# Performance work log

Measured on AMD Instinct MI355X. Metric: run time of the kernel, lower is better.

Reference implementation:

```python
import jax, jax.numpy as jnp
import numpy as np

N_NODES = 50000
N_EDGES = 1600000
D = 128


def _degree_norm(idx, n_nodes, dtype):
    # unweighted degree, clamped to >= 1, power -1/2 (DGL norm='both')
    deg = jax.ops.segment_sum(jnp.ones((idx.shape[0],), dtype=dtype), idx,
                              num_segments=n_nodes)
    return jax.lax.rsqrt(jnp.maximum(deg, 1.0))


def _graph_conv(h, e_weight, src, dst, W, b, out_norm, in_norm):
    # DGL GraphConv, norm='both', aggregate-first (in_feats == out_feats)
    feat_src = h * out_norm[:, None]                     # [N, D]
    msg = feat_src[src] * e_weight[:, None]              # [E, D] gather + edge weight
    agg = jax.ops.segment_sum(msg, dst, num_segments=h.shape[0])  # [N, D] scatter-add
    agg = agg * in_norm[:, None]
    return jax.nn.relu(agg @ W + b)


def setup_inputs() -> dict:
    key = jax.random.key(0)
    ks = jax.random.split(key, 6)
    x = jax.random.normal(ks[0], (N_NODES, D), dtype=jnp.float32)
    e_weight = jax.random.uniform(ks[1], (N_EDGES,), dtype=jnp.float32)
    src = jax.random.randint(ks[2], (N_EDGES,), 0, N_NODES)
    dst = jax.random.randint(ks[3], (N_EDGES,), 0, N_NODES)
    scale = 1.0 / np.sqrt(D)
    W1 = jax.random.normal(ks[4], (D, D), dtype=jnp.float32) * scale
    W2 = jax.random.normal(ks[5], (D, D), dtype=jnp.float32) * scale
    b1 = jnp.zeros((D,), dtype=jnp.float32)
    b2 = jnp.zeros((D,), dtype=jnp.float32)
    return {"x": x, "e_weight": e_weight, "src": src, "dst": dst,
            "W1": W1, "b1": b1, "W2": W2, "b2": b2}


def reference(x, e_weight, src, dst, W1, b1, W2, b2):
    n = x.shape[0]
    out_norm = _degree_norm(src, n, x.dtype)  # src -> out-degree norm
    in_norm = _degree_norm(dst, n, x.dtype)   # dst -> in-degree norm
    h = x
    for W, b in ((W1, b1), (W2, b2)):
        h_nxt = _graph_conv(h, e_weight, src, dst, W, b, out_norm, in_norm)
        h = h_nxt + h  # residual=1, dims match
    return h
```

## Files before the change

kernel.cpp:

```cpp
#include <hip/hip_runtime.h>

static constexpr int NN = 50000;
static constexpr int NE = 1600000;
static constexpr int DD = 128;
static constexpr int STRIDE = 72;
static constexpr int NBUCK = 196;
static constexpr int CAP = 9000;
static constexpr int B1B = 512;
static constexpr int CHUNK = NE / B1B;
static constexpr int SCAN_BLOCKS = (NN + 255) / 256;

typedef __attribute__((ext_vector_type(8))) short short8;
typedef __attribute__((ext_vector_type(4))) float f32x4;

__device__ inline unsigned short f2b(float f) {
    unsigned u = __float_as_uint(f);
    return (unsigned short)((u + 0x7FFFu + ((u >> 16) & 1u)) >> 16);
}
__device__ inline float b2f(unsigned short h) {
    return __uint_as_float(((unsigned)h) << 16);
}
__device__ inline unsigned pack2(float lo, float hi) {
    return (unsigned)f2b(lo) | ((unsigned)f2b(hi) << 16);
}
__device__ inline void acc8(float* a, uint4 r, float w) {
    a[0] = fmaf(__uint_as_float(r.x << 16), w, a[0]);
    a[1] = fmaf(__uint_as_float(r.x & 0xFFFF0000u), w, a[1]);
    a[2] = fmaf(__uint_as_float(r.y << 16), w, a[2]);
    a[3] = fmaf(__uint_as_float(r.y & 0xFFFF0000u), w, a[3]);
    a[4] = fmaf(__uint_as_float(r.z << 16), w, a[4]);
    a[5] = fmaf(__uint_as_float(r.z & 0xFFFF0000u), w, a[5]);
    a[6] = fmaf(__uint_as_float(r.w << 16), w, a[6]);
    a[7] = fmaf(__uint_as_float(r.w & 0xFFFF0000u), w, a[7]);
}


__global__ __launch_bounds__(256) void build1_kernel(
    const int* __restrict__ src, const int* __restrict__ dst,
    const float* __restrict__ ew,
    int* __restrict__ gCurD, int* __restrict__ gCurS,
    uint2* __restrict__ tempD, unsigned short* __restrict__ tempS) {
    __shared__ int lsrc[CHUNK];
    __shared__ int ldst[CHUNK];
    __shared__ int histD[NBUCK * 2], histS[NBUCK * 2];
    __shared__ int baseD[NBUCK], baseS[NBUCK];
    int tid = threadIdx.x;
    int cp = tid & 1;
    for (int i = tid; i < NBUCK; i += 256) {
        histD[i * 2] = 0; histD[i * 2 + 1] = 0;
        histS[i * 2] = 0; histS[i * 2 + 1] = 0;
    }
    int lo = blockIdx.x * CHUNK;
    for (int i = tid; i < CHUNK; i += 256) {
        lsrc[i] = src[lo + i];
        ldst[i] = dst[lo + i];
    }
    __syncthreads();
    for (int i = tid; i < CHUNK; i += 256) {
        atomicAdd(&histD[(ldst[i] >> 8) * 2 + cp], 1);
        atomicAdd(&histS[(lsrc[i] >> 8) * 2 + cp], 1);
    }
    __syncthreads();
    for (int i = tid; i < NBUCK; i += 256) {
        int d0 = histD[i * 2], d1 = histD[i * 2 + 1];
        baseD[i] = atomicAdd(&gCurD[i], d0 + d1);
        histD[i * 2] = 0; histD[i * 2 + 1] = d0;
        int s0 = histS[i * 2], s1 = histS[i * 2 + 1];
        baseS[i] = atomicAdd(&gCurS[i], s0 + s1);
        histS[i * 2] = 0; histS[i * 2 + 1] = s0;
    }
    __syncthreads();
    for (int i = tid; i < CHUNK; i += 256) {
        int s = lsrc[i], d = ldst[i];
        unsigned short wb = f2b(ew[lo + i]);
        int bd = d >> 8, bs = s >> 8;
        int pd = baseD[bd] + atomicAdd(&histD[bd * 2 + cp], 1);
        if (pd < CAP) tempD[(size_t)bd * CAP + pd] = make_uint2(((unsigned)s << 16) | wb, (unsigned)d);
        int ps = baseS[bs] + atomicAdd(&histS[bs * 2 + cp], 1);
        if (ps < CAP) tempS[(size_t)bs * CAP + ps] = (unsigned short)(s & 255);
    }
}

__global__ __launch_bounds__(512) void build2_kernel(
    const unsigned short* __restrict__ tempS, const int* __restrict__ gCurS,
    const uint2* __restrict__ tempD, const int* __restrict__ gCurD,
    const float* __restrict__ x, float* __restrict__ onorm,
    unsigned short* __restrict__ xs,
    unsigned* __restrict__ edges, int* __restrict__ cnt_in,
    float* __restrict__ inorm,
    const float* __restrict__ W1, const float* __restrict__ W2,
    unsigned short* __restrict__ Wt1, unsigned short* __restrict__ Wt2) {
    __shared__ int cur[256];
    __shared__ float on[256];
    int tid = threadIdx.x, b = blockIdx.x;

    if (b < NBUCK) {
        if (tid < 256) cur[tid] = 0;
        __syncthreads();
        int n = min(gCurS[b], CAP);
        const unsigned short* rec = tempS + (size_t)b * CAP;
        for (int i = tid; i < n; i += 512) atomicAdd(&cur[rec[i]], 1);
        __syncthreads();
        if (tid < 256) {
            int node = (b << 8) + tid;
            float o = rsqrtf(fmaxf((float)cur[tid], 1.0f));
            on[tid] = o;
            if (node < NN) onorm[node] = o;
        }
        __syncthreads();
        #pragma unroll
        for (int k = 0; k < 8; ++k) {
            int t = tid + (k << 9);
            int r = t >> 4, sub = t & 15;
            int node = (b << 8) + r;
            if (node >= NN) continue;
            const float4* xv = (const float4*)(x + (size_t)node * DD + sub * 8);
            float o = on[r];
            float4 a = xv[0], c = xv[1];
            uint4 oo;
            oo.x = pack2(a.x * o, a.y * o);
            oo.y = pack2(a.z * o, a.w * o);
            oo.z = pack2(c.x * o, c.y * o);
            oo.w = pack2(c.z * o, c.w * o);
            ((uint4*)xs)[(size_t)node * 16 + sub] = oo;
        }
    } else if (b < 2 * NBUCK) {
        int bb = b - NBUCK;
        if (tid < 256) cur[tid] = 0;
        __syncthreads();
        int n = min(gCurD[bb], CAP);
        const uint2* rec = tempD + (size_t)bb * CAP;
        for (int i = tid; i < n; i += 512) {
            uint2 r = rec[i];
            int d = (int)r.y;
            int slot = atomicAdd(&cur[d & 255], 1);
            if (slot < STRIDE) edges[(size_t)d * STRIDE + slot] = r.x;
        }
        __syncthreads();
        if (tid < 256) {
            int node = (bb << 8) + tid;
            if (node < NN) {
                int c = cur[tid];
                cnt_in[node] = min(c, STRIDE);
                inorm[node] = rsqrtf(fmaxf((float)c, 1.0f));
            }
        }
    } else {
        for (int idx = tid; idx < 2 * 16384; idx += 512) {
            const float* Ws = (idx < 16384) ? W1 : W2;
            unsigned short* Wd = (idx < 16384) ? Wt1 : Wt2;
            int i = idx & 16383;
            int k = i >> 7, n = i & 127;
            Wd[n * 128 + k] = f2b(Ws[i]);
        }
    }
}

template<bool WRITE_HS>
__global__ __launch_bounds__(256) void fused_kernel(
    const unsigned short* __restrict__ hsrc, const unsigned* __restrict__ edges,
    const int* __restrict__ cnt, const unsigned short* __restrict__ Wt,
    const float* __restrict__ bias, const float* __restrict__ inorm,
    const float* __restrict__ onorm, const float* __restrict__ hres,
    float* __restrict__ out, unsigned short* __restrict__ hs) {
    __shared__ uint4 lsA[256];

    int tid = threadIdx.x;
    int node0 = blockIdx.x * 16;

    {
        int nl = tid >> 4;
        int lane = tid & 15;
        int node = node0 + nl;
        int n = cnt[node];
        const uint4* rows = (const uint4*)hsrc;
        const unsigned* ep = edges + node * STRIDE;
        float acc[8] = {0.f,0.f,0.f,0.f,0.f,0.f,0.f,0.f};
        int i = 0;
        for (; i + 8 <= n; i += 8) {
            uint4 ea = *(const uint4*)(ep + i);
            uint4 eb = *(const uint4*)(ep + i + 4);
            uint4 r0 = rows[(ea.x >> 16) * 16 + lane];
            uint4 r1 = rows[(ea.y >> 16) * 16 + lane];
            uint4 r2 = rows[(ea.z >> 16) * 16 + lane];
            uint4 r3 = rows[(ea.w >> 16) * 16 + lane];
            uint4 r4 = rows[(eb.x >> 16) * 16 + lane];
            uint4 r5 = rows[(eb.y >> 16) * 16 + lane];
            uint4 r6 = rows[(eb.z >> 16) * 16 + lane];
            uint4 r7 = rows[(eb.w >> 16) * 16 + lane];
            acc8(acc, r0, b2f((unsigned short)(ea.x & 0xFFFFu)));
            acc8(acc, r1, b2f((unsigned short)(ea.y & 0xFFFFu)));
            acc8(acc, r2, b2f((unsigned short)(ea.z & 0xFFFFu)));
            acc8(acc, r3, b2f((unsigned short)(ea.w & 0xFFFFu)));
            acc8(acc, r4, b2f((unsigned short)(eb.x & 0xFFFFu)));
            acc8(acc, r5, b2f((unsigned short)(eb.y & 0xFFFFu)));
            acc8(acc, r6, b2f((unsigned short)(eb.z & 0xFFFFu)));
            acc8(acc, r7, b2f((unsigned short)(eb.w & 0xFFFFu)));
        }
        if (i + 4 <= n) {
            uint4 ea = *(const uint4*)(ep + i);
            uint4 r0 = rows[(ea.x >> 16) * 16 + lane];
            uint4 r1 = rows[(ea.y >> 16) * 16 + lane];
            uint4 r2 = rows[(ea.z >> 16) * 16 + lane];
            uint4 r3 = rows[(ea.w >> 16) * 16 + lane];
            acc8(acc, r0, b2f((unsigned short)(ea.x & 0xFFFFu)));
            acc8(acc, r1, b2f((unsigned short)(ea.y & 0xFFFFu)));
            acc8(acc, r2, b2f((unsigned short)(ea.z & 0xFFFFu)));
            acc8(acc, r3, b2f((unsigned short)(ea.w & 0xFFFFu)));
            i += 4;
        }
        for (; i < n; ++i) {
            unsigned wrd = ep[i];
            uint4 r = rows[(wrd >> 16) * 16 + lane];
            acc8(acc, r, b2f((unsigned short)(wrd & 0xFFFFu)));
        }
        uint4 p;
        p.x = pack2(acc[0], acc[1]);
        p.y = pack2(acc[2], acc[3]);
        p.z = pack2(acc[4], acc[5]);
        p.w = pack2(acc[6], acc[7]);
        lsA[nl * 16 + (lane ^ nl)] = p;
    }
    __syncthreads();

    int l = tid & 63;
    int w = tid >> 6;
    int r16 = l & 15;
    int q = l >> 4;

    const short8* lsAs = (const short8*)lsA;
    short8 afrag[4];
    #pragma unroll
    for (int kk = 0; kk < 4; ++kk) {
        int chunk = kk * 4 + q;
        afrag[kk] = lsAs[r16 * 16 + (chunk ^ r16)];
    }

    int col0 = w * 32 + r16;
    int col1 = col0 + 16;
    const uint4* wt4 = (const uint4*)Wt;
    f32x4 acc0 = {0.f, 0.f, 0.f, 0.f};
    f32x4 acc1 = {0.f, 0.f, 0.f, 0.f};
    #pragma unroll
    for (int kk = 0; kk < 4; ++kk) {
        int cidx = kk * 4 + q;
        uint4 bu0 = wt4[col0 * 16 + cidx];
        uint4 bu1 = wt4[col1 * 16 + cidx];
        short8 b0 = *(const short8*)&bu0;
        short8 b1 = *(const short8*)&bu1;
        acc0 = __builtin_amdgcn_mfma_f32_16x16x32_bf16(afrag[kk], b0, acc0, 0, 0, 0);
        acc1 = __builtin_amdgcn_mfma_f32_16x16x32_bf16(afrag[kk], b1, acc1, 0, 0, 0);
    }

    float bc0 = bias[col0], bc1 = bias[col1];
    #pragma unroll
    for (int reg = 0; reg < 4; ++reg) {
        int row = q * 4 + reg;
        int n = node0 + row;
        float inr = inorm[n];
        size_t o0 = (size_t)n * DD + col0;
        size_t o1 = (size_t)n * DD + col1;
        float v0 = fmaxf(fmaf(acc0[reg], inr, bc0), 0.0f) + hres[o0];
        float v1 = fmaxf(fmaf(acc1[reg], inr, bc1), 0.0f) + hres[o1];
        out[o0] = v0;
        out[o1] = v1;
        if (WRITE_HS) {
            float on = onorm[n];
            hs[o0] = f2b(v0 * on);
            hs[o1] = f2b(v1 * on);
        }
    }
}


__global__ void count_dst_kernel(const int* __restrict__ dst, int* __restrict__ cnt_dst) {
    int e = blockIdx.x * 256 + threadIdx.x;
    if (e < NE) atomicAdd(&cnt_dst[dst[e]], 1);
}

__global__ void scan1_kernel(const int* __restrict__ cnt, int* __restrict__ offs,
                             int* __restrict__ bsum) {
    __shared__ int s[256];
    int tid = threadIdx.x;
    int i = blockIdx.x * 256 + tid;
    int v = (i < NN) ? cnt[i] : 0;
    s[tid] = v;
    __syncthreads();
    #pragma unroll
    for (int off = 1; off < 256; off <<= 1) {
        int t = (tid >= off) ? s[tid - off] : 0;
        __syncthreads();
        s[tid] += t;
        __syncthreads();
    }
    if (i < NN) offs[i] = s[tid] - v;
    if (tid == 255) bsum[blockIdx.x] = s[255];
}

__global__ void scan2_kernel(int* __restrict__ bsum) {
    __shared__ int s[256];
    int tid = threadIdx.x;
    int v = (tid < SCAN_BLOCKS) ? bsum[tid] : 0;
    s[tid] = v;
    __syncthreads();
    #pragma unroll
    for (int off = 1; off < 256; off <<= 1) {
        int t = (tid >= off) ? s[tid - off] : 0;
        __syncthreads();
        s[tid] += t;
        __syncthreads();
    }
    if (tid < SCAN_BLOCKS) bsum[tid] = s[tid] - v;
}

__global__ void scan3_kernel(int* __restrict__ offs, const int* __restrict__ bsum) {
    int i = blockIdx.x * 256 + threadIdx.x;
    if (i < NN) offs[i] += bsum[blockIdx.x];
    if (i == 0) offs[NN] = NE;
}

__global__ void bucket_csr_kernel(const int* __restrict__ src, const int* __restrict__ dst,
                                  const float* __restrict__ ew, const int* __restrict__ offs,
                                  int* __restrict__ cursor, int* __restrict__ cnt_src,
                                  unsigned* __restrict__ edges) {
    int e = blockIdx.x * 256 + threadIdx.x;
    if (e >= NE) return;
    int s = src[e], d = dst[e];
    unsigned short wb = f2b(ew[e]);
    int pos = offs[d] + atomicAdd(&cursor[d], 1);
    edges[pos] = ((unsigned)s << 16) | (unsigned)wb;
    atomicAdd(&cnt_src[s], 1);
}

__global__ void norm_kernel(const int* __restrict__ cnt_src, const int* __restrict__ cursor,
                            float* __restrict__ onorm, float* __restrict__ inorm) {
    int i = blockIdx.x * 256 + threadIdx.x;
    if (i < NN) {
        onorm[i] = rsqrtf(fmaxf((float)cnt_src[i], 1.0f));
        inorm[i] = rsqrtf(fmaxf((float)cursor[i], 1.0f));
    }
}

__global__ void convert_kernel(const float* __restrict__ x, const float* __restrict__ onorm,
                               unsigned short* __restrict__ xs) {
    int idx = blockIdx.x * 256 + threadIdx.x;
    if (idx >= NN * DD / 8) return;
    const float4* xv = (const float4*)(x + (size_t)idx * 8);
    float on = onorm[idx >> 4];
    float4 a = xv[0], c = xv[1];
    uint4 o;
    o.x = pack2(a.x * on, a.y * on);
    o.y = pack2(a.z * on, a.w * on);
    o.z = pack2(c.x * on, c.y * on);
    o.w = pack2(c.z * on, c.w * on);
    ((uint4*)xs)[idx] = o;
}

template<bool PADDED>
__global__ __launch_bounds__(256) void gather_kernel(
    const unsigned short* __restrict__ hsrc, const unsigned* __restrict__ edges,
    const int* __restrict__ offs, const int* __restrict__ cnt,
    unsigned short* __restrict__ agg) {
    int t = blockIdx.x * 256 + threadIdx.x;
    int node = t >> 5;
    int lane = t & 31;
    if (node >= NN) return;
    int base = PADDED ? node * STRIDE : offs[node];
    int n = cnt[node];
    const ushort4* rows = (const ushort4*)hsrc;
    float4 acc = make_float4(0.f, 0.f, 0.f, 0.f);
    for (int i = 0; i < n; ++i) {
        unsigned wrd = edges[base + i];
        float w = b2f((unsigned short)(wrd & 0xFFFFu));
        ushort4 v = rows[(wrd >> 16) * 32 + lane];
        acc.x = fmaf(b2f(v.x), w, acc.x);
        acc.y = fmaf(b2f(v.y), w, acc.y);
        acc.z = fmaf(b2f(v.z), w, acc.z);
        acc.w = fmaf(b2f(v.w), w, acc.w);
    }
    ushort4 o;
    o.x = f2b(acc.x); o.y = f2b(acc.y); o.z = f2b(acc.z); o.w = f2b(acc.w);
    ((ushort4*)agg)[node * 32 + lane] = o;
}

template<bool WRITE_HS>
__global__ __launch_bounds__(256) void gemm_kernel(
    const unsigned short* __restrict__ agg, const float* __restrict__ inorm,
    const float* __restrict__ W, const float* __restrict__ b,
    const float* __restrict__ hres, float* __restrict__ out,
    const float* __restrict__ onorm, unsigned short* __restrict__ hs) {
    __shared__ float rows[16 * DD];

    int tid = threadIdx.x;
    int node0 = blockIdx.x * 16;

    uint4 t4 = ((const uint4*)(agg + (size_t)node0 * DD))[tid];
    int bidx = tid * 8;
    rows[bidx + 0] = b2f((unsigned short)(t4.x & 0xFFFFu));
    rows[bidx + 1] = b2f((unsigned short)(t4.x >> 16));
    rows[bidx + 2] = b2f((unsigned short)(t4.y & 0xFFFFu));
    rows[bidx + 3] = b2f((unsigned short)(t4.y >> 16));
    rows[bidx + 4] = b2f((unsigned short)(t4.z & 0xFFFFu));
    rows[bidx + 5] = b2f((unsigned short)(t4.z >> 16));
    rows[bidx + 6] = b2f((unsigned short)(t4.w & 0xFFFFu));
    rows[bidx + 7] = b2f((unsigned short)(t4.w >> 16));
    __syncthreads();

    int col = tid & 127;
    int mbase = (tid >> 7) * 8;
    float bcol = b[col];

    float acc[8] = {0.f,0.f,0.f,0.f,0.f,0.f,0.f,0.f};

    #pragma unroll 4
    for (int k = 0; k < DD; ++k) {
        float wkj = W[k * DD + col];
        #pragma unroll
        for (int m = 0; m < 8; ++m)
            acc[m] = fmaf(rows[(mbase + m) * DD + k], wkj, acc[m]);
    }

    #pragma unroll
    for (int m = 0; m < 8; ++m) {
        int n = node0 + mbase + m;
        float r = fmaxf(fmaf(acc[m], inorm[n], bcol), 0.0f) + hres[(size_t)n * DD + col];
        out[(size_t)n * DD + col] = r;
        if (WRITE_HS) hs[(size_t)n * DD + col] = f2b(r * onorm[n]);
    }
}

extern "C" void kernel_launch(void* const* d_in, const int* in_sizes, int n_in,
                              void* d_out, int out_size, void* d_ws, size_t ws_size,
                              hipStream_t stream) {
    const float* x  = (const float*)d_in[0];
    const float* ew = (const float*)d_in[1];
    const int*   src = (const int*)d_in[2];
    const int*   dst = (const int*)d_in[3];
    const float* W1 = (const float*)d_in[4];
    const float* b1 = (const float*)d_in[5];
    const float* W2 = (const float*)d_in[6];
    const float* b2 = (const float*)d_in[7];
    float* out = (float*)d_out;

    const int EB = (NE + 255) / 256;
    const int NB = (NN + 255) / 256;
    const int GB = (NN * 32 + 255) / 256;
    const int MB = NN / 16;

    size_t offA  = 0;
    size_t offT  = offA + (size_t)NN * DD * 2;
    size_t offE  = offT + (size_t)NBUCK * CAP * 8;
    size_t offI  = offE + (size_t)NN * STRIDE * 4;
    size_t need  = offI + (2 * NBUCK + 3 * NN) * sizeof(int) + 2 * 16384 * 2;

    if (ws_size >= need) {
        unsigned short* bufA = (unsigned short*)((char*)d_ws + offA);
        uint2*    tempD = (uint2*)((char*)d_ws + offT);
        unsigned short* bufC = (unsigned short*)((char*)d_ws + offT);
        unsigned* edges = (unsigned*)((char*)d_ws + offE);
        unsigned short* tempS = (unsigned short*)((char*)d_ws + offE);
        int* gCurD = (int*)((char*)d_ws + offI);
        int* gCurS = gCurD + NBUCK;
        int* cnt_in = gCurS + NBUCK;
        float* inorm = (float*)(cnt_in + NN);
        float* onorm = inorm + NN;
        unsigned short* Wt1 = (unsigned short*)(onorm + NN);
        unsigned short* Wt2 = Wt1 + 16384;

        hipMemsetAsync(gCurD, 0, 2 * NBUCK * sizeof(int), stream);
        build1_kernel<<<B1B, 256, 0, stream>>>(src, dst, ew, gCurD, gCurS, tempD, tempS);
        build2_kernel<<<2 * NBUCK + 1, 512, 0, stream>>>(
            tempS, gCurS, tempD, gCurD, x, onorm, bufA,
            edges, cnt_in, inorm, W1, W2, Wt1, Wt2);

        fused_kernel<true><<<MB, 256, 0, stream>>>(bufA, edges, cnt_in, Wt1, b1,
                                                   inorm, onorm, x, out, bufC);
        fused_kernel<false><<<MB, 256, 0, stream>>>(bufC, edges, cnt_in, Wt2, b2,
                                                    inorm, onorm, out, out, nullptr);
    } else {
        unsigned short* bufA = (unsigned short*)d_ws;
        unsigned short* bufB = bufA + (size_t)NN * DD;
        int* cnt_src = (int*)(bufB + (size_t)NN * DD);
        int* cursor  = cnt_src + NN;
        int* cnt_dst = cursor + NN;
        int* offs    = cnt_dst + NN;
        int* bsum    = offs + NN + 1;
        float* onorm = (float*)(bsum + 256);
        float* inorm = onorm + NN;
        unsigned* edges = (unsigned*)(inorm + NN);

        hipMemsetAsync(cnt_src, 0, 3 * NN * sizeof(int), stream);
        count_dst_kernel<<<EB, 256, 0, stream>>>(dst, cnt_dst);
        scan1_kernel<<<NB, 256, 0, stream>>>(cnt_dst, offs, bsum);
        scan2_kernel<<<1, 256, 0, stream>>>(bsum);
        scan3_kernel<<<NB, 256, 0, stream>>>(offs, bsum);
        bucket_csr_kernel<<<EB, 256, 0, stream>>>(src, dst, ew, offs, cursor, cnt_src, edges);
        norm_kernel<<<NB, 256, 0, stream>>>(cnt_src, cursor, onorm, inorm);
        convert_kernel<<<MB, 256, 0, stream>>>(x, onorm, bufA);

        gather_kernel<false><<<GB, 256, 0, stream>>>(bufA, edges, offs, cursor, bufB);
        gemm_kernel<true><<<MB, 256, 0, stream>>>(bufB, inorm, W1, b1, x, out, onorm, bufA);
        gather_kernel<false><<<GB, 256, 0, stream>>>(bufA, edges, offs, cursor, bufB);
        gemm_kernel<false><<<MB, 256, 0, stream>>>(bufB, inorm, W2, b2, out, out, onorm, nullptr);
    }
}
```

Measured before the change: 306.1 us.

## Split bucket records into narrower arrays and stage edge lists in shared memory

The bucketing pass now stores the destination record as a 4-byte packed src/weight word plus a 1-byte local destination index, and the source record as a single byte, instead of 8-byte and 2-byte records. It also reads src/dst directly from global memory rather than copying the chunk into LDS, and drops the two-way split histograms. The CSR build kernel splits each destination bucket across two blocks, scatters edges into a shared-memory staging area, then writes the padded edge rows out with coalesced 16-byte stores instead of scattered 4-byte global writes. Each half-bucket block rescans the whole bucket's byte array, and the workspace layout is reshuffled so edges no longer alias tempS.

```diff
diff --git a/kernel.cpp b/kernel.cpp
--- a/kernel.cpp
+++ b/kernel.cpp
@@ -39,66 +39,57 @@
     const int* __restrict__ src, const int* __restrict__ dst,
     const float* __restrict__ ew,
     int* __restrict__ gCurD, int* __restrict__ gCurS,
-    uint2* __restrict__ tempD, unsigned short* __restrict__ tempS) {
-    __shared__ int lsrc[CHUNK];
-    __shared__ int ldst[CHUNK];
-    __shared__ int histD[NBUCK * 2], histS[NBUCK * 2];
-    __shared__ int baseD[NBUCK], baseS[NBUCK];
+    unsigned* __restrict__ tempD1, unsigned char* __restrict__ tempD0,
+    unsigned char* __restrict__ tempS) {
+    __shared__ int histD[NBUCK], histS[NBUCK], baseD[NBUCK], baseS[NBUCK];
     int tid = threadIdx.x;
-    int cp = tid & 1;
+    for (int i = tid; i < NBUCK; i += 256) { histD[i] = 0; histS[i] = 0; }
+    __syncthreads();
+    int lo = blockIdx.x * CHUNK, hi = lo + CHUNK;
+    for (int i = lo + tid; i < hi; i += 256) {
+        atomicAdd(&histD[dst[i] >> 8], 1);
+        atomicAdd(&histS[src[i] >> 8], 1);
+    }
+    __syncthreads();
     for (int i = tid; i < NBUCK; i += 256) {
-        histD[i * 2] = 0; histD[i * 2 + 1] = 0;
-        histS[i * 2] = 0; histS[i * 2 + 1] = 0;
-    }
-    int lo = blockIdx.x * CHUNK;
-    for (int i = tid; i < CHUNK; i += 256) {
-        lsrc[i] = src[lo + i];
-        ldst[i] = dst[lo + i];
-    }
-    __syncthreads();
-    for (int i = tid; i < CHUNK; i += 256) {
-        atomicAdd(&histD[(ldst[i] >> 8) * 2 + cp], 1);
-        atomicAdd(&histS[(lsrc[i] >> 8) * 2 + cp], 1);
-    }
-    __syncthreads();
-    for (int i = tid; i < NBUCK; i += 256) {
-        int d0 = histD[i * 2], d1 = histD[i * 2 + 1];
-        baseD[i] = atomicAdd(&gCurD[i], d0 + d1);
-        histD[i * 2] = 0; histD[i * 2 + 1] = d0;
-        int s0 = histS[i * 2], s1 = histS[i * 2 + 1];
-        baseS[i] = atomicAdd(&gCurS[i], s0 + s1);
-        histS[i * 2] = 0; histS[i * 2 + 1] = s0;
-    }
-    __syncthreads();
-    for (int i = tid; i < CHUNK; i += 256) {
-        int s = lsrc[i], d = ldst[i];
-        unsigned short wb = f2b(ew[lo + i]);
+        baseD[i] = atomicAdd(&gCurD[i], histD[i]); histD[i] = 0;
+        baseS[i] = atomicAdd(&gCurS[i], histS[i]); histS[i] = 0;
+    }
+    __syncthreads();
+    for (int i = lo + tid; i < hi; i += 256) {
+        int s = src[i], d = dst[i];
+        unsigned short wb = f2b(ew[i]);
         int bd = d >> 8, bs = s >> 8;
-        int pd = baseD[bd] + atomicAdd(&histD[bd * 2 + cp], 1);
-        if (pd < CAP) tempD[(size_t)bd * CAP + pd] = make_uint2(((unsigned)s << 16) | wb, (unsigned)d);
-        int ps = baseS[bs] + atomicAdd(&histS[bs * 2 + cp], 1);
-        if (ps < CAP) tempS[(size_t)bs * CAP + ps] = (unsigned short)(s & 255);
+        int pd = baseD[bd] + atomicAdd(&histD[bd], 1);
+        if (pd < CAP) {
+            tempD1[(size_t)bd * CAP + pd] = ((unsigned)s << 16) | wb;
+            tempD0[(size_t)bd * CAP + pd] = (unsigned char)(d & 255);
+        }
+        int ps = baseS[bs] + atomicAdd(&histS[bs], 1);
+        if (ps < CAP) tempS[(size_t)bs * CAP + ps] = (unsigned char)(s & 255);
     }
 }
 
 __global__ __launch_bounds__(512) void build2_kernel(
-    const unsigned short* __restrict__ tempS, const int* __restrict__ gCurS,
-    const uint2* __restrict__ tempD, const int* __restrict__ gCurD,
+    const unsigned char* __restrict__ tempS, const int* __restrict__ gCurS,
+    const unsigned* __restrict__ tempD1, const unsigned char* __restrict__ tempD0,
+    const int* __restrict__ gCurD,
     const float* __restrict__ x, float* __restrict__ onorm,
     unsigned short* __restrict__ xs,
     unsigned* __restrict__ edges, int* __restrict__ cnt_in,
     float* __restrict__ inorm,
     const float* __restrict__ W1, const float* __restrict__ W2,
     unsigned short* __restrict__ Wt1, unsigned short* __restrict__ Wt2) {
-    __shared__ int cur[256];
-    __shared__ float on[256];
+    __shared__ unsigned shbuf[128 * STRIDE + 128];
     int tid = threadIdx.x, b = blockIdx.x;
 
     if (b < NBUCK) {
+        int* cur = (int*)shbuf;
+        float* on = (float*)(shbuf + 256);
         if (tid < 256) cur[tid] = 0;
         __syncthreads();
         int n = min(gCurS[b], CAP);
-        const unsigned short* rec = tempS + (size_t)b * CAP;
+        const unsigned char* rec = tempS + (size_t)b * CAP;
         for (int i = tid; i < n; i += 512) atomicAdd(&cur[rec[i]], 1);
         __syncthreads();
         if (tid < 256) {
@@ -124,21 +115,31 @@
             oo.w = pack2(c.z * o, c.w * o);
             ((uint4*)xs)[(size_t)node * 16 + sub] = oo;
         }
-    } else if (b < 2 * NBUCK) {
-        int bb = b - NBUCK;
-        if (tid < 256) cur[tid] = 0;
+    } else if (b < 3 * NBUCK) {
+        int hb = b - NBUCK;
+        int bb = hb >> 1, h = hb & 1;
+        int* cur = (int*)shbuf;
+        unsigned* stage = shbuf + 128;
+        if (tid < 128) cur[tid] = 0;
         __syncthreads();
         int n = min(gCurD[bb], CAP);
-        const uint2* rec = tempD + (size_t)bb * CAP;
+        const unsigned* r1 = tempD1 + (size_t)bb * CAP;
+        const unsigned char* r0 = tempD0 + (size_t)bb * CAP;
         for (int i = tid; i < n; i += 512) {
-            uint2 r = rec[i];
-            int d = (int)r.y;
-            int slot = atomicAdd(&cur[d & 255], 1);
-            if (slot < STRIDE) edges[(size_t)d * STRIDE + slot] = r.x;
-        }
-        __syncthreads();
-        if (tid < 256) {
-            int node = (bb << 8) + tid;
+            int dl = r0[i];
+            if ((dl >> 7) == h) {
+                int li = dl & 127;
+                int slot = atomicAdd(&cur[li], 1);
+                if (slot < STRIDE) stage[li * STRIDE + slot] = r1[i];
+            }
+        }
+        __syncthreads();
+        size_t base = ((size_t)(bb << 8) + (h << 7)) * STRIDE;
+        uint4* dv = (uint4*)(edges + base);
+        const uint4* sv = (const uint4*)stage;
+        for (int i = tid; i < 128 * STRIDE / 4; i += 512) dv[i] = sv[i];
+        if (tid < 128) {
+            int node = (bb << 8) + (h << 7) + tid;
             if (node < NN) {
                 int c = cur[tid];
                 cnt_in[node] = min(c, STRIDE);
@@ -449,16 +450,17 @@
 
     size_t offA  = 0;
     size_t offT  = offA + (size_t)NN * DD * 2;
-    size_t offE  = offT + (size_t)NBUCK * CAP * 8;
-    size_t offI  = offE + (size_t)NN * STRIDE * 4;
+    size_t offE  = offT + (size_t)NN * DD * 2;
+    size_t offI  = offE + (size_t)NBUCK * 256 * STRIDE * 4;
     size_t need  = offI + (2 * NBUCK + 3 * NN) * sizeof(int) + 2 * 16384 * 2;
 
     if (ws_size >= need) {
         unsigned short* bufA = (unsigned short*)((char*)d_ws + offA);
-        uint2*    tempD = (uint2*)((char*)d_ws + offT);
+        unsigned* tempD1 = (unsigned*)((char*)d_ws + offT);
+        unsigned char* tempD0 = (unsigned char*)((char*)d_ws + offT + (size_t)NBUCK * CAP * 4);
+        unsigned char* tempS  = (unsigned char*)((char*)d_ws + offT + (size_t)NBUCK * CAP * 5);
         unsigned short* bufC = (unsigned short*)((char*)d_ws + offT);
         unsigned* edges = (unsigned*)((char*)d_ws + offE);
-        unsigned short* tempS = (unsigned short*)((char*)d_ws + offE);
         int* gCurD = (int*)((char*)d_ws + offI);
         int* gCurS = gCurD + NBUCK;
         int* cnt_in = gCurS + NBUCK;
@@ -468,9 +470,10 @@
         unsigned short* Wt2 = Wt1 + 16384;
 
         hipMemsetAsync(gCurD, 0, 2 * NBUCK * sizeof(int), stream);
-        build1_kernel<<<B1B, 256, 0, stream>>>(src, dst, ew, gCurD, gCurS, tempD, tempS);
-        build2_kernel<<<2 * NBUCK + 1, 512, 0, stream>>>(
-            tempS, gCurS, tempD, gCurD, x, onorm, bufA,
+        build1_kernel<<<B1B, 256, 0, stream>>>(src, dst, ew, gCurD, gCurS,
+                                               tempD1, tempD0, tempS);
+        build2_kernel<<<3 * NBUCK + 1, 512, 0, stream>>>(
+            tempS, gCurS, tempD1, tempD0, gCurD, x, onorm, bufA,
             edges, cnt_in, inorm, W1, W2, Wt1, Wt2);
 
         fused_kernel<true><<<MB, 256, 0, stream>>>(bufA, edges, cnt_in, Wt1, b1,
```

Result: slower. 312.8 us (+2.2%).
